# Kernel tuning notes

Measured on AMD Instinct MI355X. Metric: run time of the kernel, lower is better.

The kernel has to match this reference:

```python
import jax, jax.numpy as jnp
import numpy as np

N = 50000       # nodes
E = 800000      # edges (avg degree 16)
F_IN = 20
HID = 500
OUT = 2
BN_EPS = 1e-5


def setup_inputs() -> dict:
    key = jax.random.key(0)
    k1, k2, k3, k4 = jax.random.split(key, 4)
    node_feature = jax.random.normal(k1, (N, F_IN), dtype=jnp.float32)
    edge_index = jax.random.randint(k2, (2, E), 0, N, dtype=jnp.int32)
    gcn_W = jax.random.normal(k3, (F_IN, HID), dtype=jnp.float32) * (1.0 / np.sqrt(F_IN))
    gcn_b = jnp.zeros((HID,), dtype=jnp.float32)
    bn_gamma = jnp.ones((HID,), dtype=jnp.float32)
    bn_beta = jnp.zeros((HID,), dtype=jnp.float32)
    lin_W = jax.random.normal(k4, (HID, OUT), dtype=jnp.float32) * (1.0 / np.sqrt(HID))
    lin_b = jnp.zeros((OUT,), dtype=jnp.float32)
    return {
        "node_feature": node_feature,
        "edge_index": edge_index,
        "gcn_W": gcn_W,
        "gcn_b": gcn_b,
        "bn_gamma": bn_gamma,
        "bn_beta": bn_beta,
        "lin_W": lin_W,
        "lin_b": lin_b,
    }


def reference(node_feature, edge_index, gcn_W, gcn_b, bn_gamma, bn_beta, lin_W, lin_b):
    n = node_feature.shape[0]
    # --- GCNConv: add self-loops, symmetric normalization, gather-scale-scatter ---
    loop = jnp.arange(n, dtype=edge_index.dtype)
    row = jnp.concatenate([edge_index[0], loop])   # sources
    col = jnp.concatenate([edge_index[1], loop])   # targets
    deg = jax.ops.segment_sum(jnp.ones(col.shape, jnp.float32), col, num_segments=n)
    dinv = jnp.where(deg > 0, jax.lax.rsqrt(jnp.maximum(deg, 1.0)), 0.0)
    norm = dinv[row] * dinv[col]                   # [E+N]
    h = node_feature @ gcn_W                       # [N, HID]
    msg = h[row] * norm[:, None]                   # [E+N, HID]
    agg = jax.ops.segment_sum(msg, col, num_segments=n) + gcn_b  # [N, HID]
    # --- BatchNorm1d (training mode: batch statistics, biased variance) ---
    mean = agg.mean(axis=0)
    var = agg.var(axis=0)
    xn = (agg - mean) * jax.lax.rsqrt(var + BN_EPS) * bn_gamma + bn_beta
    rsu_embedding = xn[0:1]                        # [1, HID]
    # --- Linear -> ReLU -> Softmax(dim=1) ---
    logits = jax.nn.relu(xn @ lin_W + lin_b)       # [N, OUT]
    action_prob = jax.nn.softmax(logits, axis=1)
    return action_prob, rsu_embedding
```

## Files before the change

kernel.cpp:

```cpp
#include <hip/hip_runtime.h>

#define F_IN 20
#define HID 500
#define N_STATS 420
#define BN_EPS 1e-5f
#define CAP 64
#define STATS_BLOCKS 128
#define NXCD 8
#define XGROUPS 256

__global__ void init_kernel(int* cnt, int n) {
    int i = blockIdx.x * blockDim.x + threadIdx.x;
    if (i < n) cnt[i] = 0;
}

__global__ void xfill_kernel(const int* __restrict__ ei, int* __restrict__ cnt,
                             unsigned short* __restrict__ srow, int E, int n) {
    int b = blockIdx.x;
    int g = b >> 3;
    int x = b & 7;
    int part = (n + NXCD - 1) / NXCD;
    int clo = x * part;
    int chi = clo + part; if (chi > n) chi = n;
    int cs = (E + XGROUPS - 1) / XGROUPS;
    int s = g * cs;
    int e_end = s + cs; if (e_end > E) e_end = E;
    for (int e = s + threadIdx.x; e < e_end; e += blockDim.x) {
        int c = ei[E + e];
        if (c >= clo && c < chi) {
            int r = ei[e];
            int p = atomicAdd(&cnt[c], 1);
            if (p < CAP) srow[(size_t)c * CAP + p] = (unsigned short)r;
        }
    }
}

__global__ void prescale_kernel(const float* __restrict__ x, const int* __restrict__ cnt,
                                float* __restrict__ y, float* __restrict__ dinv, int n) {
    int g = blockIdx.x * blockDim.x + threadIdx.x;
    int i = g / 5, c = g % 5;
    if (i >= n) return;
    float di = rsqrtf((float)(cnt[i] + 1));
    if (c == 0) dinv[i] = di;
    float4 v = *(const float4*)(x + (size_t)i * F_IN + 4 * c);
    v.x *= di; v.y *= di; v.z *= di; v.w *= di;
    *(float4*)(y + (size_t)i * F_IN + 4 * c) = v;
}

__global__ void gather_y_kernel(const float* __restrict__ y,
                                const unsigned short* __restrict__ srow,
                                const int* __restrict__ cnt, const float* __restrict__ dinv,
                                float* __restrict__ aggx, int n) {
    int g = blockIdx.x * blockDim.x + threadIdx.x;
    int i = g / 5, c = g % 5;
    if (i >= n) return;
    float di = dinv[i];
    int mi = cnt[i];
    if (mi > CAP) mi = CAP;
    float4 acc = *(const float4*)(y + (size_t)i * F_IN + 4 * c);
    const unsigned short* sp = srow + (size_t)i * CAP;
    int j = 0;
    for (; j + 8 <= mi; j += 8) {
        uint4 pk = *(const uint4*)(sp + j);
        int rr[8];
        rr[0] = pk.x & 0xffff; rr[1] = pk.x >> 16;
        rr[2] = pk.y & 0xffff; rr[3] = pk.y >> 16;
        rr[4] = pk.z & 0xffff; rr[5] = pk.z >> 16;
        rr[6] = pk.w & 0xffff; rr[7] = pk.w >> 16;
#pragma unroll
        for (int k = 0; k < 8; ++k) {
            float4 v = *(const float4*)(y + (size_t)rr[k] * F_IN + 4 * c);
            acc.x += v.x; acc.y += v.y; acc.z += v.z; acc.w += v.w;
        }
    }
    for (; j < mi; ++j) {
        int r = sp[j];
        float4 v = *(const float4*)(y + (size_t)r * F_IN + 4 * c);
        acc.x += v.x; acc.y += v.y; acc.z += v.z; acc.w += v.w;
    }
    acc.x *= di; acc.y *= di; acc.z *= di; acc.w *= di;
    *(float4*)(aggx + (size_t)i * F_IN + 4 * c) = acc;
}

#define CHUNK 128
__global__ __launch_bounds__(512) void stats_kernel(const float* __restrict__ aggx,
                                                    float* __restrict__ partial, int n) {
    __shared__ float buf[CHUNK * F_IN];
    int tid = threadIdx.x;
    float acc = 0.0f;
    int nch = (n + CHUNK - 1) / CHUNK;
    for (int ch = blockIdx.x; ch < nch; ch += gridDim.x) {
        int base = ch * CHUNK;
        for (int k = tid; k < CHUNK * F_IN; k += 512) {
            int r = base + k / F_IN;
            buf[k] = (r < n) ? aggx[(size_t)base * F_IN + k] : 0.0f;
        }
        __syncthreads();
        if (tid < 400) {
            int f1 = tid / F_IN, f2 = tid % F_IN;
            for (int r = 0; r < CHUNK; ++r)
                acc = fmaf(buf[r * F_IN + f1], buf[r * F_IN + f2], acc);
        } else if (tid < N_STATS) {
            int f = tid - 400;
            for (int r = 0; r < CHUNK; ++r) acc += buf[r * F_IN + f];
        }
        __syncthreads();
    }
    if (tid < N_STATS) partial[blockIdx.x * N_STATS + tid] = acc;
}

__global__ __launch_bounds__(512) void finalize_kernel(
    const float* __restrict__ aggx, const float* __restrict__ W, const float* __restrict__ b,
    const float* __restrict__ gamma, const float* __restrict__ beta,
    const float* __restrict__ linW, const float* __restrict__ linb,
    const float* __restrict__ partial, float* __restrict__ weff, float* __restrict__ out, int n) {
    __shared__ float mu[F_IN], M[400], a0[F_IN], sA[HID], tA[HID];
    int t = threadIdx.x;
    if (t < N_STATS) {
        float s = 0.0f;
        for (int k = 0; k < STATS_BLOCKS; ++k) s += partial[k * N_STATS + t];
        float v = s / (float)n;
        if (t < 400) M[t] = v; else mu[t - 400] = v;
    }
    if (t < F_IN) a0[t] = aggx[t];
    __syncthreads();
    if (t < HID) {
        float wv[F_IN];
#pragma unroll
        for (int f = 0; f < F_IN; ++f) wv[f] = W[f * HID + t];
        float mdot = 0.0f;
#pragma unroll
        for (int f = 0; f < F_IN; ++f) mdot = fmaf(mu[f], wv[f], mdot);
        float bj = b[t];
        float m = mdot + bj;
        float e2 = 0.0f;
        for (int f1 = 0; f1 < F_IN; ++f1) {
            float inner = 0.0f;
#pragma unroll
            for (int f2 = 0; f2 < F_IN; ++f2) inner = fmaf(M[f1 * F_IN + f2], wv[f2], inner);
            e2 = fmaf(wv[f1], inner, e2);
        }
        float ex2 = e2 + 2.0f * bj * mdot + bj * bj;
        float var = ex2 - m * m;
        float s = gamma[t] * rsqrtf(var + BN_EPS);
        float tt = beta[t] - m * s;
        sA[t] = s;
        tA[t] = tt;
        float dotv = 0.0f;
#pragma unroll
        for (int f = 0; f < F_IN; ++f) dotv = fmaf(a0[f], wv[f], dotv);
        out[2 * n + t] = (dotv + bj) * s + tt;
    }
    __syncthreads();
    if (t < 40) {
        int f = t >> 1, c = t & 1;
        float acc = 0.0f;
        for (int j = 0; j < HID; ++j)
            acc = fmaf(sA[j] * W[f * HID + j], linW[j * 2 + c], acc);
        weff[t] = acc;
    } else if (t < 42) {
        int c = t - 40;
        float acc = linb[c];
        for (int j = 0; j < HID; ++j)
            acc = fmaf(fmaf(b[j], sA[j], tA[j]), linW[j * 2 + c], acc);
        weff[40 + c] = acc;
    }
}

__global__ void output_kernel(const float* __restrict__ aggx, const float* __restrict__ weff,
                              float* __restrict__ out, int n) {
    __shared__ float wl[42];
    if (threadIdx.x < 42) wl[threadIdx.x] = weff[threadIdx.x];
    __syncthreads();
    int i = blockIdx.x * blockDim.x + threadIdx.x;
    if (i >= n) return;
    const float4* ap = (const float4*)(aggx + (size_t)i * F_IN);
    float l0 = wl[40], l1 = wl[41];
#pragma unroll
    for (int k = 0; k < 5; ++k) {
        float4 v = ap[k];
        l0 = fmaf(v.x, wl[2 * (4 * k + 0)], l0);
        l1 = fmaf(v.x, wl[2 * (4 * k + 0) + 1], l1);
        l0 = fmaf(v.y, wl[2 * (4 * k + 1)], l0);
        l1 = fmaf(v.y, wl[2 * (4 * k + 1) + 1], l1);
        l0 = fmaf(v.z, wl[2 * (4 * k + 2)], l0);
        l1 = fmaf(v.z, wl[2 * (4 * k + 2) + 1], l1);
        l0 = fmaf(v.w, wl[2 * (4 * k + 3)], l0);
        l1 = fmaf(v.w, wl[2 * (4 * k + 3) + 1], l1);
    }
    l0 = fmaxf(l0, 0.0f);
    l1 = fmaxf(l1, 0.0f);
    float mx = fmaxf(l0, l1);
    float e0 = expf(l0 - mx), e1 = expf(l1 - mx);
    float inv = 1.0f / (e0 + e1);
    float2 p = make_float2(e0 * inv, e1 * inv);
    *(float2*)(out + 2 * (size_t)i) = p;
}

__global__ void fill_slot_kernel(const int* __restrict__ ei, int* __restrict__ cnt,
                                 unsigned short* __restrict__ srow, int E) {
    int e = blockIdx.x * blockDim.x + threadIdx.x;
    if (e >= E) return;
    int r = ei[e];
    int c = ei[E + e];
    int p = atomicAdd(&cnt[c], 1);
    if (p < CAP) srow[(size_t)c * CAP + p] = (unsigned short)r;
}

__global__ void gather_slot_kernel(const float* __restrict__ x,
                                   const unsigned short* __restrict__ srow,
                                   const int* __restrict__ cnt,
                                   float* __restrict__ aggx, int n) {
    int g = blockIdx.x * blockDim.x + threadIdx.x;
    int i = g / 5, c = g % 5;
    if (i >= n) return;
    int mi = cnt[i];
    float di = rsqrtf((float)(mi + 1));
    if (mi > CAP) mi = CAP;
    float s2 = di * di;
    float4 acc = *(const float4*)(x + (size_t)i * F_IN + 4 * c);
    acc.x *= s2; acc.y *= s2; acc.z *= s2; acc.w *= s2;
    const unsigned short* sp = srow + (size_t)i * CAP;
    for (int j = 0; j < mi; ++j) {
        int r = sp[j];
        float nrm = rsqrtf((float)(cnt[r] + 1)) * di;
        float4 v = *(const float4*)(x + (size_t)r * F_IN + 4 * c);
        acc.x = fmaf(v.x, nrm, acc.x);
        acc.y = fmaf(v.y, nrm, acc.y);
        acc.z = fmaf(v.z, nrm, acc.z);
        acc.w = fmaf(v.w, nrm, acc.w);
    }
    *(float4*)(aggx + (size_t)i * F_IN + 4 * c) = acc;
}

extern "C" void kernel_launch(void* const* d_in, const int* in_sizes, int n_in,
                              void* d_out, int out_size, void* d_ws, size_t ws_size,
                              hipStream_t stream) {
    const float* x     = (const float*)d_in[0];
    const int*   ei    = (const int*)d_in[1];
    const float* W     = (const float*)d_in[2];
    const float* b     = (const float*)d_in[3];
    const float* gamma = (const float*)d_in[4];
    const float* beta  = (const float*)d_in[5];
    const float* linW  = (const float*)d_in[6];
    const float* linb  = (const float*)d_in[7];
    float* out = (float*)d_out;

    int n = in_sizes[0] / F_IN;
    int E = in_sizes[1] / 2;
    const int BT = 256;

    size_t needNew = (size_t)n * 4 * 42 + (STATS_BLOCKS * N_STATS + 64) * 4 + (size_t)n * CAP * 2 + 256;

    if (ws_size >= needNew) {
        int*   cnt     = (int*)d_ws;
        float* dinv    = (float*)(cnt + n);
        float* y       = dinv + n;
        float* aggx    = y + (size_t)F_IN * n;
        float* partial = aggx + (size_t)F_IN * n;
        float* weff    = partial + STATS_BLOCKS * N_STATS;
        unsigned short* srow = (unsigned short*)(weff + 64);

        hipLaunchKernelGGL(init_kernel, dim3((n + BT - 1) / BT), dim3(BT), 0, stream, cnt, n);
        hipLaunchKernelGGL(xfill_kernel, dim3(XGROUPS * NXCD), dim3(BT), 0, stream, ei, cnt, srow, E, n);
        hipLaunchKernelGGL(prescale_kernel, dim3((5 * n + BT - 1) / BT), dim3(BT), 0, stream, x, cnt, y, dinv, n);
        hipLaunchKernelGGL(gather_y_kernel, dim3((5 * n + BT - 1) / BT), dim3(BT), 0, stream,
                           y, srow, cnt, dinv, aggx, n);
        hipLaunchKernelGGL(stats_kernel, dim3(STATS_BLOCKS), dim3(512), 0, stream, aggx, partial, n);
        hipLaunchKernelGGL(finalize_kernel, dim3(1), dim3(512), 0, stream,
                           aggx, W, b, gamma, beta, linW, linb, partial, weff, out, n);
        hipLaunchKernelGGL(output_kernel, dim3((n + BT - 1) / BT), dim3(BT), 0, stream, aggx, weff, out, n);
    } else {
        int*   cnt     = (int*)d_ws;
        float* aggx    = (float*)(cnt + n);
        float* partial = aggx + (size_t)F_IN * n;
        float* weff    = partial + STATS_BLOCKS * N_STATS;
        unsigned short* srow = (unsigned short*)(weff + 64);

        hipLaunchKernelGGL(init_kernel, dim3((n + BT - 1) / BT), dim3(BT), 0, stream, cnt, n);
        hipLaunchKernelGGL(fill_slot_kernel, dim3((E + BT - 1) / BT), dim3(BT), 0, stream, ei, cnt, srow, E);
        hipLaunchKernelGGL(gather_slot_kernel, dim3((5 * n + BT - 1) / BT), dim3(BT), 0, stream,
                           x, srow, cnt, aggx, n);
        hipLaunchKernelGGL(stats_kernel, dim3(STATS_BLOCKS), dim3(512), 0, stream, aggx, partial, n);
        hipLaunchKernelGGL(finalize_kernel, dim3(1), dim3(512), 0, stream,
                           aggx, W, b, gamma, beta, linW, linb, partial, weff, out, n);
        hipLaunchKernelGGL(output_kernel, dim3((n + BT - 1) / BT), dim3(BT), 0, stream, aggx, weff, out, n);
    }
}
```

Measured before the change: 185.1 us.

## Fuse neighbor gather with BatchNorm covariance statistics in one kernel

Merges the gather kernel and the separate stats kernel. Each 320-thread block now aggregates 64 nodes, stages the results in shared memory and immediately computes per-block feature sums and second moments. This removes one launch and the re-read of the aggregated features. In exchange, the single-block finalize kernel must reduce about 782 partial rows instead of 128. The small-workspace fallback path is also dropped, so the code now assumes a larger workspace.

```diff
diff --git a/kernel.cpp b/kernel.cpp
--- a/kernel.cpp
+++ b/kernel.cpp
@@ -5,9 +5,10 @@
 #define N_STATS 420
 #define BN_EPS 1e-5f
 #define CAP 64
-#define STATS_BLOCKS 128
 #define NXCD 8
 #define XGROUPS 256
+#define GNODES 64
+#define GBT 320
 
 __global__ void init_kernel(int* cnt, int n) {
     int i = blockIdx.x * blockDim.x + threadIdx.x;
@@ -47,78 +48,77 @@
     *(float4*)(y + (size_t)i * F_IN + 4 * c) = v;
 }
 
-__global__ void gather_y_kernel(const float* __restrict__ y,
-                                const unsigned short* __restrict__ srow,
-                                const int* __restrict__ cnt, const float* __restrict__ dinv,
-                                float* __restrict__ aggx, int n) {
-    int g = blockIdx.x * blockDim.x + threadIdx.x;
-    int i = g / 5, c = g % 5;
-    if (i >= n) return;
-    float di = dinv[i];
-    int mi = cnt[i];
-    if (mi > CAP) mi = CAP;
-    float4 acc = *(const float4*)(y + (size_t)i * F_IN + 4 * c);
-    const unsigned short* sp = srow + (size_t)i * CAP;
-    int j = 0;
-    for (; j + 8 <= mi; j += 8) {
-        uint4 pk = *(const uint4*)(sp + j);
-        int rr[8];
-        rr[0] = pk.x & 0xffff; rr[1] = pk.x >> 16;
-        rr[2] = pk.y & 0xffff; rr[3] = pk.y >> 16;
-        rr[4] = pk.z & 0xffff; rr[5] = pk.z >> 16;
-        rr[6] = pk.w & 0xffff; rr[7] = pk.w >> 16;
-#pragma unroll
-        for (int k = 0; k < 8; ++k) {
-            float4 v = *(const float4*)(y + (size_t)rr[k] * F_IN + 4 * c);
+__global__ __launch_bounds__(GBT) void gather_stats_kernel(
+    const float* __restrict__ y, const unsigned short* __restrict__ srow,
+    const int* __restrict__ cnt, const float* __restrict__ dinv,
+    float* __restrict__ aggx, float* __restrict__ partial, int n) {
+    __shared__ float buf[GNODES * F_IN];
+    int il = threadIdx.x / 5, c = threadIdx.x % 5;
+    int i = blockIdx.x * GNODES + il;
+    float4 acc = make_float4(0.f, 0.f, 0.f, 0.f);
+    if (i < n) {
+        float di = dinv[i];
+        int mi = cnt[i];
+        if (mi > CAP) mi = CAP;
+        acc = *(const float4*)(y + (size_t)i * F_IN + 4 * c);
+        const unsigned short* sp = srow + (size_t)i * CAP;
+        int j = 0;
+        for (; j + 8 <= mi; j += 8) {
+            uint4 pk = *(const uint4*)(sp + j);
+            int rr[8];
+            rr[0] = pk.x & 0xffff; rr[1] = pk.x >> 16;
+            rr[2] = pk.y & 0xffff; rr[3] = pk.y >> 16;
+            rr[4] = pk.z & 0xffff; rr[5] = pk.z >> 16;
+            rr[6] = pk.w & 0xffff; rr[7] = pk.w >> 16;
+#pragma unroll
+            for (int k = 0; k < 8; ++k) {
+                float4 v = *(const float4*)(y + (size_t)rr[k] * F_IN + 4 * c);
+                acc.x += v.x; acc.y += v.y; acc.z += v.z; acc.w += v.w;
+            }
+        }
+        for (; j < mi; ++j) {
+            int r = sp[j];
+            float4 v = *(const float4*)(y + (size_t)r * F_IN + 4 * c);
             acc.x += v.x; acc.y += v.y; acc.z += v.z; acc.w += v.w;
         }
-    }
-    for (; j < mi; ++j) {
-        int r = sp[j];
-        float4 v = *(const float4*)(y + (size_t)r * F_IN + 4 * c);
-        acc.x += v.x; acc.y += v.y; acc.z += v.z; acc.w += v.w;
-    }
-    acc.x *= di; acc.y *= di; acc.z *= di; acc.w *= di;
-    *(float4*)(aggx + (size_t)i * F_IN + 4 * c) = acc;
-}
-
-#define CHUNK 128
-__global__ __launch_bounds__(512) void stats_kernel(const float* __restrict__ aggx,
-                                                    float* __restrict__ partial, int n) {
-    __shared__ float buf[CHUNK * F_IN];
-    int tid = threadIdx.x;
-    float acc = 0.0f;
-    int nch = (n + CHUNK - 1) / CHUNK;
-    for (int ch = blockIdx.x; ch < nch; ch += gridDim.x) {
-        int base = ch * CHUNK;
-        for (int k = tid; k < CHUNK * F_IN; k += 512) {
-            int r = base + k / F_IN;
-            buf[k] = (r < n) ? aggx[(size_t)base * F_IN + k] : 0.0f;
-        }
-        __syncthreads();
-        if (tid < 400) {
-            int f1 = tid / F_IN, f2 = tid % F_IN;
-            for (int r = 0; r < CHUNK; ++r)
-                acc = fmaf(buf[r * F_IN + f1], buf[r * F_IN + f2], acc);
-        } else if (tid < N_STATS) {
-            int f = tid - 400;
-            for (int r = 0; r < CHUNK; ++r) acc += buf[r * F_IN + f];
-        }
-        __syncthreads();
-    }
-    if (tid < N_STATS) partial[blockIdx.x * N_STATS + tid] = acc;
+        acc.x *= di; acc.y *= di; acc.z *= di; acc.w *= di;
+        *(float4*)(aggx + (size_t)i * F_IN + 4 * c) = acc;
+    }
+    *(float4*)(buf + il * F_IN + 4 * c) = acc;
+    __syncthreads();
+    float s0 = 0.f, s1 = 0.f;
+    int t = threadIdx.x;
+    {
+        int f1 = t / F_IN, f2 = t % F_IN;
+        for (int r = 0; r < GNODES; ++r)
+            s0 = fmaf(buf[r * F_IN + f1], buf[r * F_IN + f2], s0);
+    }
+    int u1 = t + GBT;
+    if (u1 < N_STATS) {
+        if (u1 < 400) {
+            int f1 = u1 / F_IN, f2 = u1 % F_IN;
+            for (int r = 0; r < GNODES; ++r)
+                s1 = fmaf(buf[r * F_IN + f1], buf[r * F_IN + f2], s1);
+        } else {
+            int f = u1 - 400;
+            for (int r = 0; r < GNODES; ++r) s1 += buf[r * F_IN + f];
+        }
+    }
+    partial[(size_t)blockIdx.x * N_STATS + t] = s0;
+    if (u1 < N_STATS) partial[(size_t)blockIdx.x * N_STATS + u1] = s1;
 }
 
 __global__ __launch_bounds__(512) void finalize_kernel(
     const float* __restrict__ aggx, const float* __restrict__ W, const float* __restrict__ b,
     const float* __restrict__ gamma, const float* __restrict__ beta,
     const float* __restrict__ linW, const float* __restrict__ linb,
-    const float* __restrict__ partial, float* __restrict__ weff, float* __restrict__ out, int n) {
+    const float* __restrict__ partial, float* __restrict__ weff, float* __restrict__ out,
+    int n, int nblocks) {
     __shared__ float mu[F_IN], M[400], a0[F_IN], sA[HID], tA[HID];
     int t = threadIdx.x;
     if (t < N_STATS) {
         float s = 0.0f;
-        for (int k = 0; k < STATS_BLOCKS; ++k) s += partial[k * N_STATS + t];
+        for (int k = 0; k < nblocks; ++k) s += partial[(size_t)k * N_STATS + t];
         float v = s / (float)n;
         if (t < 400) M[t] = v; else mu[t - 400] = v;
     }
@@ -197,42 +197,6 @@
     *(float2*)(out + 2 * (size_t)i) = p;
 }
 
-__global__ void fill_slot_kernel(const int* __restrict__ ei, int* __restrict__ cnt,
-                                 unsigned short* __restrict__ srow, int E) {
-    int e = blockIdx.x * blockDim.x + threadIdx.x;
-    if (e >= E) return;
-    int r = ei[e];
-    int c = ei[E + e];
-    int p = atomicAdd(&cnt[c], 1);
-    if (p < CAP) srow[(size_t)c * CAP + p] = (unsigned short)r;
-}
-
-__global__ void gather_slot_kernel(const float* __restrict__ x,
-                                   const unsigned short* __restrict__ srow,
-                                   const int* __restrict__ cnt,
-                                   float* __restrict__ aggx, int n) {
-    int g = blockIdx.x * blockDim.x + threadIdx.x;
-    int i = g / 5, c = g % 5;
-    if (i >= n) return;
-    int mi = cnt[i];
-    float di = rsqrtf((float)(mi + 1));
-    if (mi > CAP) mi = CAP;
-    float s2 = di * di;
-    float4 acc = *(const float4*)(x + (size_t)i * F_IN + 4 * c);
-    acc.x *= s2; acc.y *= s2; acc.z *= s2; acc.w *= s2;
-    const unsigned short* sp = srow + (size_t)i * CAP;
-    for (int j = 0; j < mi; ++j) {
-        int r = sp[j];
-        float nrm = rsqrtf((float)(cnt[r] + 1)) * di;
-        float4 v = *(const float4*)(x + (size_t)r * F_IN + 4 * c);
-        acc.x = fmaf(v.x, nrm, acc.x);
-        acc.y = fmaf(v.y, nrm, acc.y);
-        acc.z = fmaf(v.z, nrm, acc.z);
-        acc.w = fmaf(v.w, nrm, acc.w);
-    }
-    *(float4*)(aggx + (size_t)i * F_IN + 4 * c) = acc;
-}
-
 extern "C" void kernel_launch(void* const* d_in, const int* in_sizes, int n_in,
                               void* d_out, int out_size, void* d_ws, size_t ws_size,
                               hipStream_t stream) {
@@ -249,41 +213,22 @@
     int n = in_sizes[0] / F_IN;
     int E = in_sizes[1] / 2;
     const int BT = 256;
-
-    size_t needNew = (size_t)n * 4 * 42 + (STATS_BLOCKS * N_STATS + 64) * 4 + (size_t)n * CAP * 2 + 256;
-
-    if (ws_size >= needNew) {
-        int*   cnt     = (int*)d_ws;
-        float* dinv    = (float*)(cnt + n);
-        float* y       = dinv + n;
-        float* aggx    = y + (size_t)F_IN * n;
-        float* partial = aggx + (size_t)F_IN * n;
-        float* weff    = partial + STATS_BLOCKS * N_STATS;
-        unsigned short* srow = (unsigned short*)(weff + 64);
-
-        hipLaunchKernelGGL(init_kernel, dim3((n + BT - 1) / BT), dim3(BT), 0, stream, cnt, n);
-        hipLaunchKernelGGL(xfill_kernel, dim3(XGROUPS * NXCD), dim3(BT), 0, stream, ei, cnt, srow, E, n);
-        hipLaunchKernelGGL(prescale_kernel, dim3((5 * n + BT - 1) / BT), dim3(BT), 0, stream, x, cnt, y, dinv, n);
-        hipLaunchKernelGGL(gather_y_kernel, dim3((5 * n + BT - 1) / BT), dim3(BT), 0, stream,
-                           y, srow, cnt, dinv, aggx, n);
-        hipLaunchKernelGGL(stats_kernel, dim3(STATS_BLOCKS), dim3(512), 0, stream, aggx, partial, n);
-        hipLaunchKernelGGL(finalize_kernel, dim3(1), dim3(512), 0, stream,
-                           aggx, W, b, gamma, beta, linW, linb, partial, weff, out, n);
-        hipLaunchKernelGGL(output_kernel, dim3((n + BT - 1) / BT), dim3(BT), 0, stream, aggx, weff, out, n);
-    } else {
-        int*   cnt     = (int*)d_ws;
-        float* aggx    = (float*)(cnt + n);
-        float* partial = aggx + (size_t)F_IN * n;
-        float* weff    = partial + STATS_BLOCKS * N_STATS;
-        unsigned short* srow = (unsigned short*)(weff + 64);
-
-        hipLaunchKernelGGL(init_kernel, dim3((n + BT - 1) / BT), dim3(BT), 0, stream, cnt, n);
-        hipLaunchKernelGGL(fill_slot_kernel, dim3((E + BT - 1) / BT), dim3(BT), 0, stream, ei, cnt, srow, E);
-        hipLaunchKernelGGL(gather_slot_kernel, dim3((5 * n + BT - 1) / BT), dim3(BT), 0, stream,
-                           x, srow, cnt, aggx, n);
-        hipLaunchKernelGGL(stats_kernel, dim3(STATS_BLOCKS), dim3(512), 0, stream, aggx, partial, n);
-        hipLaunchKernelGGL(finalize_kernel, dim3(1), dim3(512), 0, stream,
-                           aggx, W, b, gamma, beta, linW, linb, partial, weff, out, n);
-        hipLaunchKernelGGL(output_kernel, dim3((n + BT - 1) / BT), dim3(BT), 0, stream, aggx, weff, out, n);
-    }
-}
+    int gblocks = (n + GNODES - 1) / GNODES;
+
+    int*   cnt     = (int*)d_ws;
+    float* dinv    = (float*)(cnt + n);
+    float* y       = dinv + n;
+    float* aggx    = y + (size_t)F_IN * n;
+    float* partial = aggx + (size_t)F_IN * n;
+    float* weff    = partial + (size_t)gblocks * N_STATS;
+    unsigned short* srow = (unsigned short*)(weff + 64);
+
+    hipLaunchKernelGGL(init_kernel, dim3((n + BT - 1) / BT), dim3(BT), 0, stream, cnt, n);
+    hipLaunchKernelGGL(xfill_kernel, dim3(XGROUPS * NXCD), dim3(BT), 0, stream, ei, cnt, srow, E, n);
+    hipLaunchKernelGGL(prescale_kernel, dim3((5 * n + BT - 1) / BT), dim3(BT), 0, stream, x, cnt, y, dinv, n);
+    hipLaunchKernelGGL(gather_stats_kernel, dim3(gblocks), dim3(GBT), 0, stream,
+                       y, srow, cnt, dinv, aggx, partial, n);
+    hipLaunchKernelGGL(finalize_kernel, dim3(1), dim3(512), 0, stream,
+                       aggx, W, b, gamma, beta, linW, linb, partial, weff, out, n, gblocks);
+    hipLaunchKernelGGL(output_kernel, dim3((n + BT - 1) / BT), dim3(BT), 0, stream, aggx, weff, out, n);
+}
```

Measured after the change: 349.9 us. 89.0% more time.
